# Performance work log

Measured on AMD Instinct MI355X. Metric: run time of the kernel, lower is better.

The kernel has to match this reference:

```python
import jax, jax.numpy as jnp
from jax import lax
import numpy as np

EPS = 1e-7  # keras.backend.epsilon()
DISCOUNT = 1.0

B, T, S, F = 32, 128, 64, 256  # samples, sentences, steps, features


def setup_inputs() -> dict:
    key = jax.random.key(0)
    ks = jax.random.split(key, 6)
    scale = 1.0 / np.sqrt(F)
    return {
        "x": jax.random.normal(ks[0], (B, T, S, F), dtype=jnp.float32),
        "W": jax.random.normal(ks[1], (F, F), dtype=jnp.float32) * scale,
        "W_context": jax.random.normal(ks[2], (F, F), dtype=jnp.float32) * scale,
        "W_l": jax.random.normal(ks[3], (F,), dtype=jnp.float32) * scale,
        "W_lc": jax.random.normal(ks[4], (F,), dtype=jnp.float32) * scale,
        "bl": jnp.zeros((1,), dtype=jnp.float32),
        "b": jnp.zeros((F,), dtype=jnp.float32),
        "u": jax.random.normal(ks[5], (F,), dtype=jnp.float32) * scale,
    }


def _forward(x, W, W_context, W_l, W_lc, bl, b, u):
    # x: [B, T, S, F]; scan over sentence axis T with carried context [B, F].
    def step(carry, x_):
        context, count = carry            # context: [B, F]
        context_ = context                # aggregate == 'sum'
        uit = jnp.einsum("bsf,fg->bsg", x_, W)            # [B, S, F]
        c = context_ @ W_context                            # [B, F]
        # gate: l = sigmoid(<context, W_lc> + bl broadcast over steps + <x, W_l>)
        gate_logit = (context_ @ W_lc + bl[0])[:, None] + x_ @ W_l  # [B, S]
        l = jax.nn.sigmoid(gate_logit)[..., None]           # [B, S, 1]
        uit = jnp.tanh(l * uit + (1.0 - l) * c[:, None, :] + b)
        ait = uit @ u                                        # [B, S]
        a = jnp.exp(ait)
        a = a / (jnp.sum(a, axis=1, keepdims=True) + EPS)   # masked-softmax (no mask)
        attended = jnp.einsum("bsf,bs->bf", x_, a)          # [B, F]
        new_context = context * DISCOUNT + attended
        return (new_context, count + 1.0), (attended, a, new_context)

    x_t = jnp.transpose(x, (1, 0, 2, 3))  # [T, B, S, F]
    init = (jnp.zeros((x.shape[0], x.shape[-1]), x.dtype), jnp.asarray(0.0, x.dtype))
    _, (out, weights, ctx) = lax.scan(step, init, x_t)
    output = jnp.transpose(out, (1, 0, 2))       # [B, T, F]
    context = jnp.transpose(ctx, (1, 0, 2))      # [B, T, F]
    weights = jnp.transpose(weights, (1, 0, 2))  # [B, T, S]
    return output, context, weights


def reference(x, W, W_context, W_l, W_lc, bl, b, u):
    return _forward(x, W, W_context, W_l, W_lc, bl, b, u)
```

## Files before the change

kernel.cpp:

```cpp
#include <hip/hip_runtime.h>
#include <stdint.h>

#define Tdim 128
#define Bdim 32
#define Sdim 64
#define Fdim 256

typedef unsigned short u16;
typedef short bf16x8 __attribute__((ext_vector_type(8)));
typedef float f32x4 __attribute__((ext_vector_type(4)));

#define K2     2.8853900817779268f
#define LOG2E  1.4426950408889634f

__device__ __forceinline__ u16 f2b(float f){
  union { float f; uint32_t u; } v; v.f = f;
  uint32_t u = v.u;
  if ((u & 0x7fffffffu) > 0x7f800000u) return (u16)0x7fc0;
  uint32_t r = (u + 0x7fffu + ((u >> 16) & 1u)) >> 16;
  return (u16)r;
}
__device__ __forceinline__ float b2f(u16 h){
  union { uint32_t u; float f; } v; v.u = ((uint32_t)h) << 16; return v.f;
}
__device__ __forceinline__ float b2f_lo(uint32_t w){
  union { uint32_t u; float f; } v; v.u = w << 16; return v.f;
}
__device__ __forceinline__ float b2f_hi(uint32_t w){
  union { uint32_t u; float f; } v; v.u = w & 0xffff0000u; return v.f;
}
__device__ __forceinline__ uint32_t pack2(float a, float b){
  return (uint32_t)f2b(a) | ((uint32_t)f2b(b) << 16);
}
__device__ __forceinline__ uint4 pack8(const float4 a, const float4 b){
  uint4 r;
  r.x = pack2(a.x, a.y); r.y = pack2(a.z, a.w);
  r.z = pack2(b.x, b.y); r.w = pack2(b.z, b.w);
  return r;
}

__device__ __forceinline__ void bar_lds(){
  asm volatile("s_waitcnt lgkmcnt(0)" ::: "memory");
  __builtin_amdgcn_s_barrier();
  asm volatile("" ::: "memory");
}


__global__ __launch_bounds__(256) void kt_transpose_cvt(const float* __restrict__ Wg,
                                                        u16* __restrict__ Wt){
  __shared__ u16 tile[64*66];
  int bx = blockIdx.x;
  int ti = bx >> 2, tj = bx & 3;
  int t = threadIdx.x;
#pragma unroll
  for (int i = 0; i < 16; ++i){
    int e = t*16 + i;
    int r = e >> 6, c = e & 63;
    tile[r*66 + c] = f2b(Wg[(ti*64 + r)*256 + tj*64 + c]);
  }
  __syncthreads();
#pragma unroll
  for (int i = 0; i < 16; ++i){
    int e = t*16 + i;
    int r = e >> 6, c = e & 63;
    Wt[(tj*64 + r)*256 + ti*64 + c] = tile[c*66 + r];
  }
}

__global__ __launch_bounds__(512, 4) void kt_gemm2(const float* __restrict__ Xg,
                                                   const u16* __restrict__ Wt,
                                                   const float* __restrict__ Wlg,
                                                   u16* __restrict__ Pg,
                                                   float* __restrict__ qg){
  __shared__ u16 Ws[256*72];
  __shared__ u16 Xs[128*72];
  __shared__ float Wls[256];
  int t  = threadIdx.x;
  int r0 = blockIdx.x * 128;
  if (t < 256) Wls[t] = Wlg[t];
  int lane = t & 63, wv = t >> 6;
  int goff = (wv & 3)*64, roff = (wv >> 2)*64;
  int fr = lane & 15, fq = lane >> 4;
  f32x4 acc[4][4];
#pragma unroll
  for (int a = 0; a < 4; ++a)
#pragma unroll
    for (int b = 0; b < 4; ++b)
      acc[a][b] = (f32x4){0.f,0.f,0.f,0.f};
  float qacc = 0.f;

  for (int kk = 0; kk < 4; ++kk){
    int k0 = kk*64;
    __syncthreads();
#pragma unroll
    for (int uu = 0; uu < 4; ++uu){
      int unit = uu*512 + t;
      int row = unit >> 3, c = unit & 7;
      *(uint4*)&Ws[row*72 + c*8] = *(const uint4*)&Wt[row*256 + k0 + c*8];
    }
#pragma unroll
    for (int uu = 0; uu < 2; ++uu){
      int unit = uu*512 + t;
      int row = unit >> 3, c = unit & 7;
      const float4* xp = (const float4*)&Xg[(size_t)(r0+row)*256 + k0 + c*8];
      *(uint4*)&Xs[row*72 + c*8] = pack8(xp[0], xp[1]);
    }
    __syncthreads();
    if (t < 128){
      int r = t;
#pragma unroll
      for (int c = 0; c < 8; ++c){
        uint4 xv = *(const uint4*)&Xs[r*72 + c*8];
        const uint32_t* xw = (const uint32_t*)&xv;
#pragma unroll
        for (int p = 0; p < 4; ++p){
          qacc = fmaf(b2f_lo(xw[p]), Wls[k0 + c*8 + 2*p],     qacc);
          qacc = fmaf(b2f_hi(xw[p]), Wls[k0 + c*8 + 2*p + 1], qacc);
        }
      }
    }
#pragma unroll
    for (int ks = 0; ks < 64; ks += 32){
      bf16x8 af[4], bf_[4];
#pragma unroll
      for (int mi = 0; mi < 4; ++mi)
        af[mi] = *(const bf16x8*)&Ws[(goff + mi*16 + fr)*72 + ks + fq*8];
#pragma unroll
      for (int ni = 0; ni < 4; ++ni)
        bf_[ni] = *(const bf16x8*)&Xs[(roff + ni*16 + fr)*72 + ks + fq*8];
#pragma unroll
      for (int mi = 0; mi < 4; ++mi)
#pragma unroll
        for (int ni = 0; ni < 4; ++ni)
          acc[mi][ni] = __builtin_amdgcn_mfma_f32_16x16x32_bf16(
              af[mi], bf_[ni], acc[mi][ni], 0, 0, 0);
    }
  }
#pragma unroll
  for (int mi = 0; mi < 4; ++mi){
    int g = goff + mi*16 + fq*4;
    int grp = g >> 4;
#pragma unroll
    for (int ni = 0; ni < 4; ++ni){
      int r = r0 + roff + ni*16 + fr;
      int bt = r >> 6, s = r & 63;
      ushort4 st;
      st.x = f2b(acc[mi][ni][0]); st.y = f2b(acc[mi][ni][1]);
      st.z = f2b(acc[mi][ni][2]); st.w = f2b(acc[mi][ni][3]);
      *(ushort4*)&Pg[(size_t)bt*16384 + grp*1024 + s*16 + fq*4] = st;
    }
  }
  if (t < 128) qg[r0 + t] = qacc;
}

__global__ __launch_bounds__(1024, 4) void kt_scan6(
    const float* __restrict__ Xg, const u16* __restrict__ Pf,
    const float* __restrict__ qf, const float* __restrict__ Wcg,
    const float* __restrict__ Wlcg, const float* __restrict__ blg,
    const float* __restrict__ biasg, const float* __restrict__ ug,
    float* __restrict__ out)
{
  __shared__ float ctx_s[256], bbr_s[256], ur_s[256], wlc_s[256];
  __shared__ float pp[64*17];
  __shared__ float attp[16*260];
  __shared__ float glc_p[4];

  const int tid   = threadIdx.x;
  const int b     = blockIdx.x;
  const int lane  = tid & 63;
  const int wave  = tid >> 6;
  const int g_loc = lane >> 2;
  const int fc    = lane & 3;
  const int gcol  = wave*16 + g_loc;
  const int f     = tid & 255;

  uint32_t wcp2[32];
#pragma unroll
  for (int i = 0; i < 16; ++i){
    int m  = (4*fc + i) & 15;
    int fb = fc*64 + m*4;
    wcp2[2*i]   = pack2(Wcg[(fb+0)*256 + gcol], Wcg[(fb+1)*256 + gcol]);
    wcp2[2*i+1] = pack2(Wcg[(fb+2)*256 + gcol], Wcg[(fb+3)*256 + gcol]);
  }

  if (tid < 256){
    ctx_s[tid] = 0.f;
    bbr_s[tid] = K2 * biasg[tid];
    ur_s[tid]  = ug[tid];
    wlc_s[tid] = Wlcg[tid];
  }
  if (tid < 4) glc_p[tid] = 0.f;
  const float blf = blg[0];
  float glcr = 0.f;

  const u16*    pP = Pf + (size_t)(b*Tdim)*16384 + wave*1024 + lane*16;
  const float4* pX = (const float4*)Xg + (size_t)(b*Tdim)*4096 + wave*256 + lane;
  const float*  pq = qf + (size_t)(b*Tdim)*64 + lane;

  uint32_t pw[8];
  {
    const uint4* pp_ = (const uint4*)pP;
    *(uint4*)&pw[0] = pp_[0]; *(uint4*)&pw[4] = pp_[1];
  }
  float qcur = pq[0];

  float* outO = out;
  float* outC = out + Bdim*Tdim*Fdim;
  float* outW = out + 2*Bdim*Tdim*Fdim;
  __syncthreads();

  for (int tt = 0; tt < Tdim; ++tt){
    const int bt    = b*Tdim + tt;
    const int nstep = (tt < Tdim-1) ? 1 : 0;

    uint32_t pwn[8];
    {
      const uint4* pp_ = (const uint4*)(pP + (size_t)nstep*16384);
      *(uint4*)&pwn[0] = pp_[0]; *(uint4*)&pwn[4] = pp_[1];
    }
    float qn = pq[nstep*64];
    float4 x0 = pX[0], x1 = pX[64], x2 = pX[128], x3 = pX[192];

    {
      glcr += glc_p[0] + glc_p[1] + glc_p[2] + glc_p[3];
      float logit = glcr + blf + qcur;
      float sig = __builtin_amdgcn_rcpf(1.f + __builtin_exp2f(-LOG2E*logit));
      const float l2  = K2 * sig;
      const float l2b = K2 - K2*sig;

      float pa = 0.f;
#pragma unroll
      for (int i = 0; i < 16; ++i){
        int m = (4*fc + i) & 15;
        float4 cv = *(const float4*)&ctx_s[fc*64 + m*4];
        pa = fmaf(cv.x, b2f_lo(wcp2[2*i]),   pa);
        pa = fmaf(cv.y, b2f_hi(wcp2[2*i]),   pa);
        pa = fmaf(cv.z, b2f_lo(wcp2[2*i+1]), pa);
        pa = fmaf(cv.w, b2f_hi(wcp2[2*i+1]), pa);
      }
      pa += __shfl_xor(pa, 1, 64);
      pa += __shfl_xor(pa, 2, 64);
      float c[16];
#pragma unroll
      for (int j = 0; j < 16; ++j)
        c[j] = __shfl(pa, 4*j, 64);

      float ait = 0.f;
#pragma unroll
      for (int j = 0; j < 16; ++j){
        float pv = (j & 1) ? b2f_hi(pw[j>>1]) : b2f_lo(pw[j>>1]);
        float bb = bbr_s[wave*16 + j];
        float uu = ur_s[wave*16 + j];
        float z  = fmaf(l2, pv, fmaf(l2b, c[j], bb));
        float e  = __builtin_exp2f(z);
        float r  = __builtin_amdgcn_rcpf(e + 1.f);
        ait += fmaf(-2.f*uu, r, uu);
      }
      pp[lane*17 + wave] = ait;
    }
    bar_lds();

    {
      const int ppb = lane*17;
      float ait = 0.f;
#pragma unroll
      for (int k = 0; k < 16; ++k) ait += pp[ppb + k];
      float mx = ait;
#pragma unroll
      for (int off = 32; off > 0; off >>= 1)
        mx = fmaxf(mx, __shfl_xor(mx, off, 64));
      float e = __builtin_exp2f(LOG2E*(ait - mx));
      float ssum = e;
#pragma unroll
      for (int off = 32; off > 0; off >>= 1)
        ssum += __shfl_xor(ssum, off, 64);
      float denom = ssum + 1e-7f * __builtin_exp2f(-LOG2E*mx);
      float a = e * __builtin_amdgcn_rcpf(denom);
      if (wave == 0) outW[(size_t)bt*Sdim + lane] = a;

      const float av0 = __shfl(a, wave*4 + 0, 64);
      const float av1 = __shfl(a, wave*4 + 1, 64);
      const float av2 = __shfl(a, wave*4 + 2, 64);
      const float av3 = __shfl(a, wave*4 + 3, 64);
      float4 acc;
      acc.x = av0*x0.x; acc.y = av0*x0.y; acc.z = av0*x0.z; acc.w = av0*x0.w;
      acc.x = fmaf(av1, x1.x, acc.x); acc.y = fmaf(av1, x1.y, acc.y);
      acc.z = fmaf(av1, x1.z, acc.z); acc.w = fmaf(av1, x1.w, acc.w);
      acc.x = fmaf(av2, x2.x, acc.x); acc.y = fmaf(av2, x2.y, acc.y);
      acc.z = fmaf(av2, x2.z, acc.z); acc.w = fmaf(av2, x2.w, acc.w);
      acc.x = fmaf(av3, x3.x, acc.x); acc.y = fmaf(av3, x3.y, acc.y);
      acc.z = fmaf(av3, x3.z, acc.z); acc.w = fmaf(av3, x3.w, acc.w);
      *(float4*)&attp[wave*260 + lane*4] = acc;
    }
    bar_lds();

    if (tid < 256){
      float att = 0.f;
#pragma unroll
      for (int k = 0; k < 16; ++k) att += attp[k*260 + f];
      const size_t o = (size_t)bt*Fdim + f;
      outO[o] = att;
      float nc = ctx_s[f] + att;
      ctx_s[f] = nc;
      outC[o] = nc;
      float gp = att * wlc_s[f];
#pragma unroll
      for (int off = 32; off > 0; off >>= 1)
        gp += __shfl_xor(gp, off, 64);
      if (lane == 0) glc_p[wave] = gp;
    }
    bar_lds();

#pragma unroll
    for (int k = 0; k < 8; ++k) pw[k] = pwn[k];
    qcur = qn;
    pP += (size_t)nstep*16384;
    pX += 4096;
    pq += 64;
  }
}

__global__ __launch_bounds__(1024) void fused_ctx_attn(
    const float* __restrict__ Xg, const float* __restrict__ Wg,
    const float* __restrict__ Wcg, const float* __restrict__ Wlg,
    const float* __restrict__ Wlcg, const float* __restrict__ blg,
    const float* __restrict__ biasg, const float* __restrict__ ug,
    float* __restrict__ out)
{
  __shared__ u16   xs[64*272];
  __shared__ float ps[64*257];
  __shared__ float cpart[8*258];
  __shared__ float qp[64*5];
  __shared__ float pp[64*17];
  __shared__ float attp[4*260];
  __shared__ float ctx_s[256], c_s[256], bb_s[256], u_s[256], wlc_s[256], wl_s[256];
  __shared__ float l2_s[64], l2b_s[64], a_s[64];
  __shared__ float glc_p[4];

  const int tid  = threadIdx.x;
  const int b    = blockIdx.x;
  const int lane = tid & 63;
  const int wave = tid >> 6;
  const int fr   = lane & 15;
  const int fq   = lane >> 4;
  const int f    = tid & 255;
  const int sb   = tid >> 8;

  bf16x8 afW[8];
  {
    const int gcol = wave*16 + fr;
#pragma unroll
    for (int kt = 0; kt < 8; ++kt){
      u16 tmp[8];
#pragma unroll
      for (int j = 0; j < 8; ++j)
        tmp[j] = f2b(Wg[(kt*32 + fq*8 + j)*256 + gcol]);
      afW[kt] = *(const bf16x8*)tmp;
    }
  }
  const int fj = tid >> 7;
  const int gp = tid & 127;
  uint32_t wcp[32];
#pragma unroll
  for (int fi = 0; fi < 32; ++fi)
    wcp[fi] = pack2(Wcg[(fj*32 + fi)*256 + gp*2], Wcg[(fj*32 + fi)*256 + gp*2 + 1]);

  if (tid < 256){
    ctx_s[tid] = 0.f;
    bb_s[tid]  = K2 * biasg[tid];
    u_s[tid]   = ug[tid];
    wlc_s[tid] = Wlcg[tid];
    wl_s[tid]  = Wlg[tid];
  }
  if (tid < 4) glc_p[tid] = 0.f;
  const float blf = blg[0];
  float glcr = 0.f;

  float* outO = out;
  float* outC = out + Bdim*Tdim*Fdim;
  float* outW = out + 2*Bdim*Tdim*Fdim;

  const int srow = tid >> 5;
  const int sc8  = (tid & 31)*8;
  {
    const long xb = (long)(b*Tdim)*Sdim*Fdim;
    const float4* p0 = (const float4*)&Xg[xb + (long)srow*256 + sc8];
    const float4* p1 = (const float4*)&Xg[xb + (long)(srow+32)*256 + sc8];
    *(uint4*)&xs[srow*272 + sc8]      = pack8(p0[0], p0[1]);
    *(uint4*)&xs[(srow+32)*272 + sc8] = pack8(p1[0], p1[1]);
  }
  __syncthreads();

  for (int tt = 0; tt < Tdim; ++tt){
    const int tn = (tt < Tdim-1) ? (tt+1) : tt;
    const long xb = (long)((b*Tdim + tn))*Sdim*Fdim;
    const float4* p0 = (const float4*)&Xg[xb + (long)srow*256 + sc8];
    const float4* p1 = (const float4*)&Xg[xb + (long)(srow+32)*256 + sc8];
    uint4 xr0 = pack8(p0[0], p0[1]);
    uint4 xr1 = pack8(p1[0], p1[1]);

    {
      float pa = 0.f, pb = 0.f;
#pragma unroll
      for (int fi = 0; fi < 32; ++fi){
        float cf = ctx_s[fj*32 + fi];
        pa = fmaf(cf, b2f_lo(wcp[fi]), pa);
        pb = fmaf(cf, b2f_hi(wcp[fi]), pb);
      }
      float2 st; st.x = pa; st.y = pb;
      *(float2*)&cpart[fj*258 + gp*2] = st;
    }
    {
      f32x4 acc[4];
#pragma unroll
      for (int nt = 0; nt < 4; ++nt) acc[nt] = (f32x4){0.f,0.f,0.f,0.f};
#pragma unroll
      for (int kt = 0; kt < 8; ++kt){
#pragma unroll
        for (int nt = 0; nt < 4; ++nt){
          bf16x8 bfx = *(const bf16x8*)&xs[(nt*16 + fr)*272 + kt*32 + fq*8];
          acc[nt] = __builtin_amdgcn_mfma_f32_16x16x32_bf16(afW[kt], bfx, acc[nt], 0, 0, 0);
        }
      }
#pragma unroll
      for (int nt = 0; nt < 4; ++nt){
        const int s = nt*16 + fr;
        const int g = wave*16 + fq*4;
        ps[s*257 + g + 0] = acc[nt][0];
        ps[s*257 + g + 1] = acc[nt][1];
        ps[s*257 + g + 2] = acc[nt][2];
        ps[s*257 + g + 3] = acc[nt][3];
      }
    }
    if (tid < 256){
      const int s = tid >> 2, qtr = tid & 3;
      float a = 0.f;
#pragma unroll
      for (int j = 0; j < 64; ++j)
        a = fmaf(b2f(xs[s*272 + qtr*64 + j]), wl_s[qtr*64 + j], a);
      qp[s*5 + qtr] = a;
    }
    __syncthreads();

    if (tid < 256){
      float a = 0.f;
#pragma unroll
      for (int k = 0; k < 8; ++k) a += cpart[k*258 + tid];
      c_s[tid] = a;
    }
    if (tid < 64){
      glcr += glc_p[0] + glc_p[1] + glc_p[2] + glc_p[3];
      float q = qp[tid*5] + qp[tid*5+1] + qp[tid*5+2] + qp[tid*5+3];
      float logit = glcr + blf + q;
      float sig = 1.f / (1.f + __builtin_exp2f(-LOG2E*logit));
      l2_s[tid]  = K2 * sig;
      l2b_s[tid] = K2 - K2*sig;
    }
    __syncthreads();

    {
      const float cf = c_s[f], bbf = bb_s[f], uf = u_s[f], n2 = -2.f*u_s[f];
#pragma unroll
      for (int i = 0; i < 16; ++i){
        const int s = sb*16 + i;
        float z2 = fmaf(l2_s[s], ps[s*257 + f], fmaf(l2b_s[s], cf, bbf));
        float e  = __builtin_exp2f(z2);
        float r  = 1.f / (e + 1.f);
        ps[s*257 + f] = fmaf(n2, r, uf);
      }
    }
    __syncthreads();

    {
      const int s = tid & 63, grp = tid >> 6;
      float a = 0.f;
#pragma unroll
      for (int k = 0; k < 16; ++k) a += ps[s*257 + grp*16 + k];
      pp[s*17 + grp] = a;
    }
    __syncthreads();

    if (tid < 64){
      const int s = tid;
      float ait = 0.f;
#pragma unroll
      for (int k = 0; k < 16; ++k) ait += pp[s*17 + k];
      float m = ait;
#pragma unroll
      for (int off = 32; off > 0; off >>= 1)
        m = fmaxf(m, __shfl_xor(m, off, 64));
      float e = __builtin_exp2f(LOG2E*(ait - m));
      float ssum = e;
#pragma unroll
      for (int off = 32; off > 0; off >>= 1)
        ssum += __shfl_xor(ssum, off, 64);
      float denom = ssum + 1e-7f * __builtin_exp2f(-LOG2E*m);
      float a = e / denom;
      a_s[s] = a;
      outW[(b*Tdim + tt)*Sdim + s] = a;
    }
    __syncthreads();

    {
      float ap = 0.f;
#pragma unroll
      for (int i = 0; i < 16; ++i){
        const int s = sb*16 + i;
        ap = fmaf(a_s[s], b2f(xs[s*272 + f]), ap);
      }
      attp[sb*260 + f] = ap;
    }
    __syncthreads();

    if (tid < 256){
      float att = attp[f] + attp[260+f] + attp[520+f] + attp[780+f];
      const int o = (b*Tdim + tt)*Fdim + f;
      outO[o] = att;
      float nc = ctx_s[f] + att;
      ctx_s[f] = nc;
      outC[o] = nc;
      float gpart = att * wlc_s[f];
#pragma unroll
      for (int off = 32; off > 0; off >>= 1)
        gpart += __shfl_xor(gpart, off, 64);
      if (lane == 0) glc_p[wave] = gpart;
    }
    *(uint4*)&xs[srow*272 + sc8] = xr0;
    *(uint4*)&xs[(srow+32)*272 + sc8] = xr1;
    __syncthreads();
  }
}

extern "C" void kernel_launch(void* const* d_in, const int* in_sizes, int n_in,
                              void* d_out, int out_size, void* d_ws, size_t ws_size,
                              hipStream_t stream){
  const float* x    = (const float*)d_in[0];
  const float* W    = (const float*)d_in[1];
  const float* Wc   = (const float*)d_in[2];
  const float* Wl   = (const float*)d_in[3];
  const float* Wlc  = (const float*)d_in[4];
  const float* bl   = (const float*)d_in[5];
  const float* bias = (const float*)d_in[6];
  const float* u    = (const float*)d_in[7];
  float* out = (float*)d_out;

  const size_t P_BYTES  = (size_t)4096*16384*2;
  const size_t Q_BYTES  = (size_t)262144*4;
  const size_t WT_BYTES = (size_t)256*256*2;
  const size_t NEED = P_BYTES + Q_BYTES + WT_BYTES;

  if (ws_size >= NEED){
    uint8_t* ws = (uint8_t*)d_ws;
    u16*   P  = (u16*)ws;
    float* q  = (float*)(ws + P_BYTES);
    u16*   Wt = (u16*)(ws + P_BYTES + Q_BYTES);
    kt_transpose_cvt<<<16, 256, 0, stream>>>(W, Wt);
    kt_gemm2<<<2048, 512, 0, stream>>>(x, Wt, Wl, P, q);
    kt_scan6<<<Bdim, 1024, 0, stream>>>(x, P, q, Wc, Wlc, bl, bias, u, out);
  } else {
    fused_ctx_attn<<<Bdim, 1024, 0, stream>>>(x, W, Wc, Wl, Wlc, bl, bias, u, out);
  }
}
```

Before: 1.082 ms.

## Fuse x·W GEMM into the sequential scan kernel with double-buffered LDS tiles

Drops the separate transpose and precompute-GEMM kernels and the large bf16 intermediate buffer. A single 32-block kernel now computes x·W per timestep with MFMA from register-resident W fragments and a double-buffered bf16 x tile in LDS, and computes the W_l gate term while loading the next tile. This removes writing and re-reading roughly 134MB of intermediate data, but puts all GEMM work on only 32 workgroups inside the serial time loop, so wide parallelism across the GPU is lost. The softmax also drops its max subtraction.

```diff
diff --git a/kernel.cpp b/kernel.cpp
--- a/kernel.cpp
+++ b/kernel.cpp
@@ -20,9 +20,6 @@
   uint32_t r = (u + 0x7fffu + ((u >> 16) & 1u)) >> 16;
   return (u16)r;
 }
-__device__ __forceinline__ float b2f(u16 h){
-  union { uint32_t u; float f; } v; v.u = ((uint32_t)h) << 16; return v.f;
-}
 __device__ __forceinline__ float b2f_lo(uint32_t w){
   union { uint32_t u; float f; } v; v.u = w << 16; return v.f;
 }
@@ -45,142 +42,51 @@
   asm volatile("" ::: "memory");
 }
 
-
-__global__ __launch_bounds__(256) void kt_transpose_cvt(const float* __restrict__ Wg,
-                                                        u16* __restrict__ Wt){
-  __shared__ u16 tile[64*66];
-  int bx = blockIdx.x;
-  int ti = bx >> 2, tj = bx & 3;
-  int t = threadIdx.x;
-#pragma unroll
-  for (int i = 0; i < 16; ++i){
-    int e = t*16 + i;
-    int r = e >> 6, c = e & 63;
-    tile[r*66 + c] = f2b(Wg[(ti*64 + r)*256 + tj*64 + c]);
-  }
-  __syncthreads();
-#pragma unroll
-  for (int i = 0; i < 16; ++i){
-    int e = t*16 + i;
-    int r = e >> 6, c = e & 63;
-    Wt[(tj*64 + r)*256 + ti*64 + c] = tile[c*66 + r];
-  }
-}
-
-__global__ __launch_bounds__(512, 4) void kt_gemm2(const float* __restrict__ Xg,
-                                                   const u16* __restrict__ Wt,
-                                                   const float* __restrict__ Wlg,
-                                                   u16* __restrict__ Pg,
-                                                   float* __restrict__ qg){
-  __shared__ u16 Ws[256*72];
-  __shared__ u16 Xs[128*72];
-  __shared__ float Wls[256];
-  int t  = threadIdx.x;
-  int r0 = blockIdx.x * 128;
-  if (t < 256) Wls[t] = Wlg[t];
-  int lane = t & 63, wv = t >> 6;
-  int goff = (wv & 3)*64, roff = (wv >> 2)*64;
-  int fr = lane & 15, fq = lane >> 4;
-  f32x4 acc[4][4];
-#pragma unroll
-  for (int a = 0; a < 4; ++a)
-#pragma unroll
-    for (int b = 0; b < 4; ++b)
-      acc[a][b] = (f32x4){0.f,0.f,0.f,0.f};
-  float qacc = 0.f;
-
-  for (int kk = 0; kk < 4; ++kk){
-    int k0 = kk*64;
-    __syncthreads();
-#pragma unroll
-    for (int uu = 0; uu < 4; ++uu){
-      int unit = uu*512 + t;
-      int row = unit >> 3, c = unit & 7;
-      *(uint4*)&Ws[row*72 + c*8] = *(const uint4*)&Wt[row*256 + k0 + c*8];
-    }
-#pragma unroll
-    for (int uu = 0; uu < 2; ++uu){
-      int unit = uu*512 + t;
-      int row = unit >> 3, c = unit & 7;
-      const float4* xp = (const float4*)&Xg[(size_t)(r0+row)*256 + k0 + c*8];
-      *(uint4*)&Xs[row*72 + c*8] = pack8(xp[0], xp[1]);
-    }
-    __syncthreads();
-    if (t < 128){
-      int r = t;
-#pragma unroll
-      for (int c = 0; c < 8; ++c){
-        uint4 xv = *(const uint4*)&Xs[r*72 + c*8];
-        const uint32_t* xw = (const uint32_t*)&xv;
-#pragma unroll
-        for (int p = 0; p < 4; ++p){
-          qacc = fmaf(b2f_lo(xw[p]), Wls[k0 + c*8 + 2*p],     qacc);
-          qacc = fmaf(b2f_hi(xw[p]), Wls[k0 + c*8 + 2*p + 1], qacc);
-        }
-      }
-    }
-#pragma unroll
-    for (int ks = 0; ks < 64; ks += 32){
-      bf16x8 af[4], bf_[4];
-#pragma unroll
-      for (int mi = 0; mi < 4; ++mi)
-        af[mi] = *(const bf16x8*)&Ws[(goff + mi*16 + fr)*72 + ks + fq*8];
-#pragma unroll
-      for (int ni = 0; ni < 4; ++ni)
-        bf_[ni] = *(const bf16x8*)&Xs[(roff + ni*16 + fr)*72 + ks + fq*8];
-#pragma unroll
-      for (int mi = 0; mi < 4; ++mi)
-#pragma unroll
-        for (int ni = 0; ni < 4; ++ni)
-          acc[mi][ni] = __builtin_amdgcn_mfma_f32_16x16x32_bf16(
-              af[mi], bf_[ni], acc[mi][ni], 0, 0, 0);
-    }
-  }
-#pragma unroll
-  for (int mi = 0; mi < 4; ++mi){
-    int g = goff + mi*16 + fq*4;
-    int grp = g >> 4;
-#pragma unroll
-    for (int ni = 0; ni < 4; ++ni){
-      int r = r0 + roff + ni*16 + fr;
-      int bt = r >> 6, s = r & 63;
-      ushort4 st;
-      st.x = f2b(acc[mi][ni][0]); st.y = f2b(acc[mi][ni][1]);
-      st.z = f2b(acc[mi][ni][2]); st.w = f2b(acc[mi][ni][3]);
-      *(ushort4*)&Pg[(size_t)bt*16384 + grp*1024 + s*16 + fq*4] = st;
-    }
-  }
-  if (t < 128) qg[r0 + t] = qacc;
-}
-
-__global__ __launch_bounds__(1024, 4) void kt_scan6(
-    const float* __restrict__ Xg, const u16* __restrict__ Pf,
-    const float* __restrict__ qf, const float* __restrict__ Wcg,
+__global__ __launch_bounds__(1024, 4) void kt_fused(
+    const float* __restrict__ Xg, const float* __restrict__ Wg,
+    const float* __restrict__ Wcg, const float* __restrict__ Wlg,
     const float* __restrict__ Wlcg, const float* __restrict__ blg,
     const float* __restrict__ biasg, const float* __restrict__ ug,
     float* __restrict__ out)
 {
-  __shared__ float ctx_s[256], bbr_s[256], ur_s[256], wlc_s[256];
+  __shared__ u16   xs[2][64*272];
   __shared__ float pp[64*17];
+  __shared__ float qp[64*17];
   __shared__ float attp[16*260];
+  __shared__ float ctx_s[256], bbr_s[256], ur_s[256], wlc_s[256], wl_s[256];
   __shared__ float glc_p[4];
 
-  const int tid   = threadIdx.x;
-  const int b     = blockIdx.x;
-  const int lane  = tid & 63;
-  const int wave  = tid >> 6;
+  const int tid  = threadIdx.x;
+  const int b    = blockIdx.x;
+  const int lane = tid & 63;
+  const int wave = tid >> 6;
+  const int fr   = lane & 15;
+  const int fq   = lane >> 4;
+  const int f    = tid & 255;
+
+  bf16x8 afW[8];
+  {
+    const int gcol = wave*16 + fr;
+#pragma unroll
+    for (int kt = 0; kt < 8; ++kt){
+      u16 tmp[8];
+#pragma unroll
+      for (int j = 0; j < 8; ++j)
+        tmp[j] = f2b(Wg[(kt*32 + fq*8 + j)*256 + gcol]);
+      afW[kt] = *(const bf16x8*)tmp;
+    }
+  }
+
   const int g_loc = lane >> 2;
   const int fc    = lane & 3;
-  const int gcol  = wave*16 + g_loc;
-  const int f     = tid & 255;
-
+  const int gcolC = wave*16 + g_loc;
   uint32_t wcp2[32];
 #pragma unroll
   for (int i = 0; i < 16; ++i){
     int m  = (4*fc + i) & 15;
     int fb = fc*64 + m*4;
-    wcp2[2*i]   = pack2(Wcg[(fb+0)*256 + gcol], Wcg[(fb+1)*256 + gcol]);
-    wcp2[2*i+1] = pack2(Wcg[(fb+2)*256 + gcol], Wcg[(fb+3)*256 + gcol]);
+    wcp2[2*i]   = pack2(Wcg[(fb+0)*256 + gcolC], Wcg[(fb+1)*256 + gcolC]);
+    wcp2[2*i+1] = pack2(Wcg[(fb+2)*256 + gcolC], Wcg[(fb+3)*256 + gcolC]);
   }
 
   if (tid < 256){
@@ -188,109 +94,137 @@
     bbr_s[tid] = K2 * biasg[tid];
     ur_s[tid]  = ug[tid];
     wlc_s[tid] = Wlcg[tid];
+    wl_s[tid]  = Wlg[tid];
   }
   if (tid < 4) glc_p[tid] = 0.f;
   const float blf = blg[0];
   float glcr = 0.f;
 
-  const u16*    pP = Pf + (size_t)(b*Tdim)*16384 + wave*1024 + lane*16;
-  const float4* pX = (const float4*)Xg + (size_t)(b*Tdim)*4096 + wave*256 + lane;
-  const float*  pq = qf + (size_t)(b*Tdim)*64 + lane;
-
-  uint32_t pw[8];
-  {
-    const uint4* pp_ = (const uint4*)pP;
-    *(uint4*)&pw[0] = pp_[0]; *(uint4*)&pw[4] = pp_[1];
-  }
-  float qcur = pq[0];
-
   float* outO = out;
   float* outC = out + Bdim*Tdim*Fdim;
   float* outW = out + 2*Bdim*Tdim*Fdim;
+
+  const int srow = tid >> 4;
+  const int sc   = (tid & 15) * 16;
+  const float4* xbase = (const float4*)(Xg) + (size_t)(b*Tdim)*4096
+                        + srow*64 + (sc >> 2);
+
   __syncthreads();
 
+  {
+    const float4* p = xbase;
+    float4 a0 = p[0], a1 = p[1], a2 = p[2], a3 = p[3];
+    *(uint4*)&xs[0][srow*272 + sc]     = pack8(a0, a1);
+    *(uint4*)&xs[0][srow*272 + sc + 8] = pack8(a2, a3);
+    float4 w0 = *(const float4*)&wl_s[sc];
+    float4 w1 = *(const float4*)&wl_s[sc + 4];
+    float4 w2 = *(const float4*)&wl_s[sc + 8];
+    float4 w3 = *(const float4*)&wl_s[sc + 12];
+    float qpart = 0.f;
+    qpart = fmaf(a0.x,w0.x, fmaf(a0.y,w0.y, fmaf(a0.z,w0.z, fmaf(a0.w,w0.w, qpart))));
+    qpart = fmaf(a1.x,w1.x, fmaf(a1.y,w1.y, fmaf(a1.z,w1.z, fmaf(a1.w,w1.w, qpart))));
+    qpart = fmaf(a2.x,w2.x, fmaf(a2.y,w2.y, fmaf(a2.z,w2.z, fmaf(a2.w,w2.w, qpart))));
+    qpart = fmaf(a3.x,w3.x, fmaf(a3.y,w3.y, fmaf(a3.z,w3.z, fmaf(a3.w,w3.w, qpart))));
+    qp[srow*17 + (tid & 15)] = qpart;
+  }
+  __syncthreads();
+
   for (int tt = 0; tt < Tdim; ++tt){
-    const int bt    = b*Tdim + tt;
-    const int nstep = (tt < Tdim-1) ? 1 : 0;
-
-    uint32_t pwn[8];
+    const int bt  = b*Tdim + tt;
+    const int tn  = (tt < Tdim-1) ? tt+1 : tt;
+    const int cur = tt & 1, nxt = cur ^ 1;
+
+    glcr += glc_p[0] + glc_p[1] + glc_p[2] + glc_p[3];
+    float qv = 0.f;
+#pragma unroll
+    for (int k = 0; k < 16; ++k) qv += qp[lane*17 + k];
+    float logit = glcr + blf + qv;
+    float sig = __builtin_amdgcn_rcpf(1.f + __builtin_exp2f(-LOG2E*logit));
+    float l2 = K2 * sig;
+    float l2sv[4];
+    l2sv[0] = __shfl(l2, fr,      64);
+    l2sv[1] = __shfl(l2, 16 + fr, 64);
+    l2sv[2] = __shfl(l2, 32 + fr, 64);
+    l2sv[3] = __shfl(l2, 48 + fr, 64);
+
+    f32x4 acc[4];
+#pragma unroll
+    for (int nt = 0; nt < 4; ++nt) acc[nt] = (f32x4){0.f,0.f,0.f,0.f};
+#pragma unroll
+    for (int kt = 0; kt < 8; ++kt){
+#pragma unroll
+      for (int nt = 0; nt < 4; ++nt){
+        bf16x8 bfx = *(const bf16x8*)&xs[cur][(nt*16 + fr)*272 + kt*32 + fq*8];
+        acc[nt] = __builtin_amdgcn_mfma_f32_16x16x32_bf16(afW[kt], bfx, acc[nt], 0, 0, 0);
+      }
+    }
+
+    float pa = 0.f;
+#pragma unroll
+    for (int i = 0; i < 16; ++i){
+      int m = (4*fc + i) & 15;
+      float4 cv = *(const float4*)&ctx_s[fc*64 + m*4];
+      pa = fmaf(cv.x, b2f_lo(wcp2[2*i]),   pa);
+      pa = fmaf(cv.y, b2f_hi(wcp2[2*i]),   pa);
+      pa = fmaf(cv.z, b2f_lo(wcp2[2*i+1]), pa);
+      pa = fmaf(cv.w, b2f_hi(wcp2[2*i+1]), pa);
+    }
+    pa += __shfl_xor(pa, 1, 64);
+    pa += __shfl_xor(pa, 2, 64);
+    float c4[4];
+#pragma unroll
+    for (int r = 0; r < 4; ++r)
+      c4[r] = __shfl(pa, 16*fq + 4*r, 64);
+    const float4 bb4 = *(const float4*)&bbr_s[wave*16 + fq*4];
+    const float4 uu4 = *(const float4*)&ur_s[wave*16 + fq*4];
+    const float* bbp = (const float*)&bb4;
+    const float* uup = (const float*)&uu4;
+
+#pragma unroll
+    for (int nt = 0; nt < 4; ++nt){
+      const float l2v  = l2sv[nt];
+      const float l2bv = K2 - l2v;
+      float ap = 0.f;
+#pragma unroll
+      for (int r = 0; r < 4; ++r){
+        float z  = fmaf(l2v, acc[nt][r], fmaf(l2bv, c4[r], bbp[r]));
+        float e  = __builtin_exp2f(z);
+        float rc = __builtin_amdgcn_rcpf(e + 1.f);
+        ap += fmaf(-2.f*uup[r], rc, uup[r]);
+      }
+      ap += __shfl_xor(ap, 16, 64);
+      ap += __shfl_xor(ap, 32, 64);
+      if (fq == 0) pp[(nt*16 + fr)*17 + wave] = ap;
+    }
+    bar_lds();
+
+    float ait = 0.f;
+#pragma unroll
+    for (int k = 0; k < 16; ++k) ait += pp[lane*17 + k];
+    float e = __builtin_exp2f(LOG2E*ait);
+    float ssum = e;
+#pragma unroll
+    for (int off = 32; off > 0; off >>= 1)
+      ssum += __shfl_xor(ssum, off, 64);
+    float a = e * __builtin_amdgcn_rcpf(ssum + 1e-7f);
+    if (wave == 0) outW[(size_t)bt*Sdim + lane] = a;
+
+    const float4* pnx = xbase + (size_t)tn*4096;
+    float4 xr0 = pnx[0], xr1 = pnx[1], xr2 = pnx[2], xr3 = pnx[3];
+
     {
-      const uint4* pp_ = (const uint4*)(pP + (size_t)nstep*16384);
-      *(uint4*)&pwn[0] = pp_[0]; *(uint4*)&pwn[4] = pp_[1];
-    }
-    float qn = pq[nstep*64];
-    float4 x0 = pX[0], x1 = pX[64], x2 = pX[128], x3 = pX[192];
-
-    {
-      glcr += glc_p[0] + glc_p[1] + glc_p[2] + glc_p[3];
-      float logit = glcr + blf + qcur;
-      float sig = __builtin_amdgcn_rcpf(1.f + __builtin_exp2f(-LOG2E*logit));
-      const float l2  = K2 * sig;
-      const float l2b = K2 - K2*sig;
-
-      float pa = 0.f;
-#pragma unroll
-      for (int i = 0; i < 16; ++i){
-        int m = (4*fc + i) & 15;
-        float4 cv = *(const float4*)&ctx_s[fc*64 + m*4];
-        pa = fmaf(cv.x, b2f_lo(wcp2[2*i]),   pa);
-        pa = fmaf(cv.y, b2f_hi(wcp2[2*i]),   pa);
-        pa = fmaf(cv.z, b2f_lo(wcp2[2*i+1]), pa);
-        pa = fmaf(cv.w, b2f_hi(wcp2[2*i+1]), pa);
+      float4 acc4 = make_float4(0.f,0.f,0.f,0.f);
+#pragma unroll
+      for (int i = 0; i < 4; ++i){
+        const int s = wave*4 + i;
+        const float av = __shfl(a, s, 64);
+        uint2 xv = *(const uint2*)&xs[cur][s*272 + lane*4];
+        acc4.x = fmaf(av, b2f_lo(xv.x), acc4.x);
+        acc4.y = fmaf(av, b2f_hi(xv.x), acc4.y);
+        acc4.z = fmaf(av, b2f_lo(xv.y), acc4.z);
+        acc4.w = fmaf(av, b2f_hi(xv.y), acc4.w);
       }
-      pa += __shfl_xor(pa, 1, 64);
-      pa += __shfl_xor(pa, 2, 64);
-      float c[16];
-#pragma unroll
-      for (int j = 0; j < 16; ++j)
-        c[j] = __shfl(pa, 4*j, 64);
-
-      float ait = 0.f;
-#pragma unroll
-      for (int j = 0; j < 16; ++j){
-        float pv = (j & 1) ? b2f_hi(pw[j>>1]) : b2f_lo(pw[j>>1]);
-        float bb = bbr_s[wave*16 + j];
-        float uu = ur_s[wave*16 + j];
-        float z  = fmaf(l2, pv, fmaf(l2b, c[j], bb));
-        float e  = __builtin_exp2f(z);
-        float r  = __builtin_amdgcn_rcpf(e + 1.f);
-        ait += fmaf(-2.f*uu, r, uu);
-      }
-      pp[lane*17 + wave] = ait;
-    }
-    bar_lds();
-
-    {
-      const int ppb = lane*17;
-      float ait = 0.f;
-#pragma unroll
-      for (int k = 0; k < 16; ++k) ait += pp[ppb + k];
-      float mx = ait;
-#pragma unroll
-      for (int off = 32; off > 0; off >>= 1)
-        mx = fmaxf(mx, __shfl_xor(mx, off, 64));
-      float e = __builtin_exp2f(LOG2E*(ait - mx));
-      float ssum = e;
-#pragma unroll
-      for (int off = 32; off > 0; off >>= 1)
-        ssum += __shfl_xor(ssum, off, 64);
-      float denom = ssum + 1e-7f * __builtin_exp2f(-LOG2E*mx);
-      float a = e * __builtin_amdgcn_rcpf(denom);
-      if (wave == 0) outW[(size_t)bt*Sdim + lane] = a;
-
-      const float av0 = __shfl(a, wave*4 + 0, 64);
-      const float av1 = __shfl(a, wave*4 + 1, 64);
-      const float av2 = __shfl(a, wave*4 + 2, 64);
-      const float av3 = __shfl(a, wave*4 + 3, 64);
-      float4 acc;
-      acc.x = av0*x0.x; acc.y = av0*x0.y; acc.z = av0*x0.z; acc.w = av0*x0.w;
-      acc.x = fmaf(av1, x1.x, acc.x); acc.y = fmaf(av1, x1.y, acc.y);
-      acc.z = fmaf(av1, x1.z, acc.z); acc.w = fmaf(av1, x1.w, acc.w);
-      acc.x = fmaf(av2, x2.x, acc.x); acc.y = fmaf(av2, x2.y, acc.y);
-      acc.z = fmaf(av2, x2.z, acc.z); acc.w = fmaf(av2, x2.w, acc.w);
-      acc.x = fmaf(av3, x3.x, acc.x); acc.y = fmaf(av3, x3.y, acc.y);
-      acc.z = fmaf(av3, x3.z, acc.z); acc.w = fmaf(av3, x3.w, acc.w);
-      *(float4*)&attp[wave*260 + lane*4] = acc;
+      *(float4*)&attp[wave*260 + lane*4] = acc4;
     }
     bar_lds();
 
@@ -309,225 +243,21 @@
         gp += __shfl_xor(gp, off, 64);
       if (lane == 0) glc_p[wave] = gp;
     }
+    *(uint4*)&xs[nxt][srow*272 + sc]     = pack8(xr0, xr1);
+    *(uint4*)&xs[nxt][srow*272 + sc + 8] = pack8(xr2, xr3);
+    {
+      float4 w0 = *(const float4*)&wl_s[sc];
+      float4 w1 = *(const float4*)&wl_s[sc + 4];
+      float4 w2 = *(const float4*)&wl_s[sc + 8];
+      float4 w3 = *(const float4*)&wl_s[sc + 12];
+      float qpart = 0.f;
+      qpart = fmaf(xr0.x,w0.x, fmaf(xr0.y,w0.y, fmaf(xr0.z,w0.z, fmaf(xr0.w,w0.w, qpart))));
+      qpart = fmaf(xr1.x,w1.x, fmaf(xr1.y,w1.y, fmaf(xr1.z,w1.z, fmaf(xr1.w,w1.w, qpart))));
+      qpart = fmaf(xr2.x,w2.x, fmaf(xr2.y,w2.y, fmaf(xr2.z,w2.z, fmaf(xr2.w,w2.w, qpart))));
+      qpart = fmaf(xr3.x,w3.x, fmaf(xr3.y,w3.y, fmaf(xr3.z,w3.z, fmaf(xr3.w,w3.w, qpart))));
+      qp[srow*17 + (tid & 15)] = qpart;
+    }
     bar_lds();
-
-#pragma unroll
-    for (int k = 0; k < 8; ++k) pw[k] = pwn[k];
-    qcur = qn;
-    pP += (size_t)nstep*16384;
-    pX += 4096;
-    pq += 64;
-  }
-}
-
-__global__ __launch_bounds__(1024) void fused_ctx_attn(
-    const float* __restrict__ Xg, const float* __restrict__ Wg,
-    const float* __restrict__ Wcg, const float* __restrict__ Wlg,
-    const float* __restrict__ Wlcg, const float* __restrict__ blg,
-    const float* __restrict__ biasg, const float* __restrict__ ug,
-    float* __restrict__ out)
-{
-  __shared__ u16   xs[64*272];
-  __shared__ float ps[64*257];
-  __shared__ float cpart[8*258];
-  __shared__ float qp[64*5];
-  __shared__ float pp[64*17];
-  __shared__ float attp[4*260];
-  __shared__ float ctx_s[256], c_s[256], bb_s[256], u_s[256], wlc_s[256], wl_s[256];
-  __shared__ float l2_s[64], l2b_s[64], a_s[64];
-  __shared__ float glc_p[4];
-
-  const int tid  = threadIdx.x;
-  const int b    = blockIdx.x;
-  const int lane = tid & 63;
-  const int wave = tid >> 6;
-  const int fr   = lane & 15;
-  const int fq   = lane >> 4;
-  const int f    = tid & 255;
-  const int sb   = tid >> 8;
-
-  bf16x8 afW[8];
-  {
-    const int gcol = wave*16 + fr;
-#pragma unroll
-    for (int kt = 0; kt < 8; ++kt){
-      u16 tmp[8];
-#pragma unroll
-      for (int j = 0; j < 8; ++j)
-        tmp[j] = f2b(Wg[(kt*32 + fq*8 + j)*256 + gcol]);
-      afW[kt] = *(const bf16x8*)tmp;
-    }
-  }
-  const int fj = tid >> 7;
-  const int gp = tid & 127;
-  uint32_t wcp[32];
-#pragma unroll
-  for (int fi = 0; fi < 32; ++fi)
-    wcp[fi] = pack2(Wcg[(fj*32 + fi)*256 + gp*2], Wcg[(fj*32 + fi)*256 + gp*2 + 1]);
-
-  if (tid < 256){
-    ctx_s[tid] = 0.f;
-    bb_s[tid]  = K2 * biasg[tid];
-    u_s[tid]   = ug[tid];
-    wlc_s[tid] = Wlcg[tid];
-    wl_s[tid]  = Wlg[tid];
-  }
-  if (tid < 4) glc_p[tid] = 0.f;
-  const float blf = blg[0];
-  float glcr = 0.f;
-
-  float* outO = out;
-  float* outC = out + Bdim*Tdim*Fdim;
-  float* outW = out + 2*Bdim*Tdim*Fdim;
-
-  const int srow = tid >> 5;
-  const int sc8  = (tid & 31)*8;
-  {
-    const long xb = (long)(b*Tdim)*Sdim*Fdim;
-    const float4* p0 = (const float4*)&Xg[xb + (long)srow*256 + sc8];
-    const float4* p1 = (const float4*)&Xg[xb + (long)(srow+32)*256 + sc8];
-    *(uint4*)&xs[srow*272 + sc8]      = pack8(p0[0], p0[1]);
-    *(uint4*)&xs[(srow+32)*272 + sc8] = pack8(p1[0], p1[1]);
-  }
-  __syncthreads();
-
-  for (int tt = 0; tt < Tdim; ++tt){
-    const int tn = (tt < Tdim-1) ? (tt+1) : tt;
-    const long xb = (long)((b*Tdim + tn))*Sdim*Fdim;
-    const float4* p0 = (const float4*)&Xg[xb + (long)srow*256 + sc8];
-    const float4* p1 = (const float4*)&Xg[xb + (long)(srow+32)*256 + sc8];
-    uint4 xr0 = pack8(p0[0], p0[1]);
-    uint4 xr1 = pack8(p1[0], p1[1]);
-
-    {
-      float pa = 0.f, pb = 0.f;
-#pragma unroll
-      for (int fi = 0; fi < 32; ++fi){
-        float cf = ctx_s[fj*32 + fi];
-        pa = fmaf(cf, b2f_lo(wcp[fi]), pa);
-        pb = fmaf(cf, b2f_hi(wcp[fi]), pb);
-      }
-      float2 st; st.x = pa; st.y = pb;
-      *(float2*)&cpart[fj*258 + gp*2] = st;
-    }
-    {
-      f32x4 acc[4];
-#pragma unroll
-      for (int nt = 0; nt < 4; ++nt) acc[nt] = (f32x4){0.f,0.f,0.f,0.f};
-#pragma unroll
-      for (int kt = 0; kt < 8; ++kt){
-#pragma unroll
-        for (int nt = 0; nt < 4; ++nt){
-          bf16x8 bfx = *(const bf16x8*)&xs[(nt*16 + fr)*272 + kt*32 + fq*8];
-          acc[nt] = __builtin_amdgcn_mfma_f32_16x16x32_bf16(afW[kt], bfx, acc[nt], 0, 0, 0);
-        }
-      }
-#pragma unroll
-      for (int nt = 0; nt < 4; ++nt){
-        const int s = nt*16 + fr;
-        const int g = wave*16 + fq*4;
-        ps[s*257 + g + 0] = acc[nt][0];
-        ps[s*257 + g + 1] = acc[nt][1];
-        ps[s*257 + g + 2] = acc[nt][2];
-        ps[s*257 + g + 3] = acc[nt][3];
-      }
-    }
-    if (tid < 256){
-      const int s = tid >> 2, qtr = tid & 3;
-      float a = 0.f;
-#pragma unroll
-      for (int j = 0; j < 64; ++j)
-        a = fmaf(b2f(xs[s*272 + qtr*64 + j]), wl_s[qtr*64 + j], a);
-      qp[s*5 + qtr] = a;
-    }
-    __syncthreads();
-
-    if (tid < 256){
-      float a = 0.f;
-#pragma unroll
-      for (int k = 0; k < 8; ++k) a += cpart[k*258 + tid];
-      c_s[tid] = a;
-    }
-    if (tid < 64){
-      glcr += glc_p[0] + glc_p[1] + glc_p[2] + glc_p[3];
-      float q = qp[tid*5] + qp[tid*5+1] + qp[tid*5+2] + qp[tid*5+3];
-      float logit = glcr + blf + q;
-      float sig = 1.f / (1.f + __builtin_exp2f(-LOG2E*logit));
-      l2_s[tid]  = K2 * sig;
-      l2b_s[tid] = K2 - K2*sig;
-    }
-    __syncthreads();
-
-    {
-      const float cf = c_s[f], bbf = bb_s[f], uf = u_s[f], n2 = -2.f*u_s[f];
-#pragma unroll
-      for (int i = 0; i < 16; ++i){
-        const int s = sb*16 + i;
-        float z2 = fmaf(l2_s[s], ps[s*257 + f], fmaf(l2b_s[s], cf, bbf));
-        float e  = __builtin_exp2f(z2);
-        float r  = 1.f / (e + 1.f);
-        ps[s*257 + f] = fmaf(n2, r, uf);
-      }
-    }
-    __syncthreads();
-
-    {
-      const int s = tid & 63, grp = tid >> 6;
-      float a = 0.f;
-#pragma unroll
-      for (int k = 0; k < 16; ++k) a += ps[s*257 + grp*16 + k];
-      pp[s*17 + grp] = a;
-    }
-    __syncthreads();
-
-    if (tid < 64){
-      const int s = tid;
-      float ait = 0.f;
-#pragma unroll
-      for (int k = 0; k < 16; ++k) ait += pp[s*17 + k];
-      float m = ait;
-#pragma unroll
-      for (int off = 32; off > 0; off >>= 1)
-        m = fmaxf(m, __shfl_xor(m, off, 64));
-      float e = __builtin_exp2f(LOG2E*(ait - m));
-      float ssum = e;
-#pragma unroll
-      for (int off = 32; off > 0; off >>= 1)
-        ssum += __shfl_xor(ssum, off, 64);
-      float denom = ssum + 1e-7f * __builtin_exp2f(-LOG2E*m);
-      float a = e / denom;
-      a_s[s] = a;
-      outW[(b*Tdim + tt)*Sdim + s] = a;
-    }
-    __syncthreads();
-
-    {
-      float ap = 0.f;
-#pragma unroll
-      for (int i = 0; i < 16; ++i){
-        const int s = sb*16 + i;
-        ap = fmaf(a_s[s], b2f(xs[s*272 + f]), ap);
-      }
-      attp[sb*260 + f] = ap;
-    }
-    __syncthreads();
-
-    if (tid < 256){
-      float att = attp[f] + attp[260+f] + attp[520+f] + attp[780+f];
-      const int o = (b*Tdim + tt)*Fdim + f;
-      outO[o] = att;
-      float nc = ctx_s[f] + att;
-      ctx_s[f] = nc;
-      outC[o] = nc;
-      float gpart = att * wlc_s[f];
-#pragma unroll
-      for (int off = 32; off > 0; off >>= 1)
-        gpart += __shfl_xor(gpart, off, 64);
-      if (lane == 0) glc_p[wave] = gpart;
-    }
-    *(uint4*)&xs[srow*272 + sc8] = xr0;
-    *(uint4*)&xs[(srow+32)*272 + sc8] = xr1;
-    __syncthreads();
   }
 }
 
@@ -543,21 +273,7 @@
   const float* bias = (const float*)d_in[6];
   const float* u    = (const float*)d_in[7];
   float* out = (float*)d_out;
-
-  const size_t P_BYTES  = (size_t)4096*16384*2;
-  const size_t Q_BYTES  = (size_t)262144*4;
-  const size_t WT_BYTES = (size_t)256*256*2;
-  const size_t NEED = P_BYTES + Q_BYTES + WT_BYTES;
-
-  if (ws_size >= NEED){
-    uint8_t* ws = (uint8_t*)d_ws;
-    u16*   P  = (u16*)ws;
-    float* q  = (float*)(ws + P_BYTES);
-    u16*   Wt = (u16*)(ws + P_BYTES + Q_BYTES);
-    kt_transpose_cvt<<<16, 256, 0, stream>>>(W, Wt);
-    kt_gemm2<<<2048, 512, 0, stream>>>(x, Wt, Wl, P, q);
-    kt_scan6<<<Bdim, 1024, 0, stream>>>(x, P, q, Wc, Wlc, bl, bias, u, out);
-  } else {
-    fused_ctx_attn<<<Bdim, 1024, 0, stream>>>(x, W, Wc, Wl, Wlc, bl, bias, u, out);
-  }
-}
+  (void)d_ws; (void)ws_size;
+
+  kt_fused<<<Bdim, 1024, 0, stream>>>(x, W, Wc, Wl, Wlc, bl, bias, u, out);
+}
```

Measured after the change: 1.790 ms. 65.4% more time.
